# Optimization experiments

Measured on AMD Instinct MI355X. Metric: run time of the kernel, lower is better.

The kernel has to match this reference:

```python
import jax, jax.numpy as jnp
import numpy as np

ALPHA = 0.1
BETA = 0.3
MARGIN = 2.0


def setup_inputs() -> dict:
    key = jax.random.key(0)
    k1, k2 = jax.random.split(key)
    prediction = jax.random.normal(k1, (8, 2048, 512), dtype=jnp.float32)
    target_seg = jax.random.randint(k2, (8, 2048), 0, 16, dtype=jnp.int64)
    return {"prediction": prediction, "target_seg": target_seg}


def _pairwise_sqdist(x):
    # x: [n, L, d] -> squared Euclidean distances [n, L, L] via a GEMM
    sq = jnp.sum(x * x, axis=-1)  # [n, L]
    inner = jnp.einsum('nld,nmd->nlm', x, x)  # [n, L, L]
    d2 = sq[:, :, None] + sq[:, None, :] - 2.0 * inner
    return jnp.maximum(d2, 0.0)


def _safe_sqrt(d2):
    # sqrt with zero (not NaN) gradient at 0, matching torch.cdist behavior
    pos = d2 > 0
    return jnp.where(pos, jnp.sqrt(jnp.where(pos, d2, 1.0)), 0.0)


def reference(prediction, target_seg):
    # y[i,j,k] = 1 if target_seg[i,j] == target_seg[i,k]
    y = (target_seg[:, :, None] == target_seg[:, None, :]).astype(prediction.dtype)
    d2 = _pairwise_sqdist(prediction)
    dist = _safe_sqrt(d2)
    hinge = jnp.maximum(MARGIN - dist, 0.0)
    loss = ALPHA * y * d2 + BETA * (1.0 - y) * hinge * hinge
    return jnp.mean(loss)
```

## Files before the change

### kernel.cpp

```cpp
#include <hip/hip_runtime.h>
#include <hip/hip_fp8.h>
#include <math.h>

#define L      2048
#define DDIM   512
#define NBATCH 8
#define BM     128
#define BN     128
#define BK     128
#define NST    (DDIM / BK)
#define NTILE  (L / BM)
#define NPAIR  (NTILE * (NTILE + 1) / 2)
#define TOTAL_BLOCKS (NBATCH * NPAIR)

#define ALPHA  0.1f
#define BETA   0.3f
#define MARGIN 2.0f

typedef __attribute__((ext_vector_type(16))) float f32x16;
typedef _Float16 f16x8 __attribute__((ext_vector_type(8)));

#define BOFF   16384

#define GLOAD_LDS16(g, l) __builtin_amdgcn_global_load_lds(              \
    (const __attribute__((address_space(1))) unsigned int*)(g),          \
    (__attribute__((address_space(3))) unsigned int*)(l), 16, 0, 0)

__global__ __launch_bounds__(256) void conv_kernel(const float* __restrict__ pred,
                                                   unsigned char* __restrict__ h,
                                                   float* __restrict__ sq) {
    int w     = threadIdx.x >> 6;
    int lane  = threadIdx.x & 63;
    int batch = blockIdx.x & 7;
    int idx   = blockIdx.x >> 3;
    int row   = batch * L + idx * 4 + w;
    const float* p = pred + (size_t)row * DDIM + lane * 8;
    float4 v0 = *(const float4*)(p);
    float4 v1 = *(const float4*)(p + 4);
    float vals[8] = {v0.x, v0.y, v0.z, v0.w, v1.x, v1.y, v1.z, v1.w};
    unsigned q[8];
    float s = 0.0f;
    #pragma unroll
    for (int i = 0; i < 8; ++i) {
        float x = vals[i];
        s = fmaf(x, x, s);
        __hip_fp8_e4m3 f8(x);
        q[i] = (unsigned)f8.__x;
    }
    unsigned lo = q[0] | (q[1] << 8) | (q[2] << 16) | (q[3] << 24);
    unsigned hi = q[4] | (q[5] << 8) | (q[6] << 16) | (q[7] << 24);
    *(uint2*)(h + (size_t)row * DDIM + lane * 8) = make_uint2(lo, hi);
    #pragma unroll
    for (int off = 32; off > 0; off >>= 1) s += __shfl_down(s, off);
    if (lane == 0) sq[row] = s;
}

__global__ __launch_bounds__(256) void loss_kernel(
        const unsigned char* __restrict__ h,
        const int*   __restrict__ seg,
        const float* __restrict__ sq,
        double*      __restrict__ partials) {
    __shared__ unsigned char smem[32768];
    __shared__ double wred[4];

    int bid = blockIdx.x;
    int n = bid & 7;
    int p = bid >> 3;
    int tj = 0;
    while (true) {
        int rl2 = NTILE - tj;
        if (p < rl2) break;
        p -= rl2;
        ++tj;
    }
    int tk = tj + p;
    int j0 = tj * BM, k0 = tk * BN;

    int t    = threadIdx.x;
    int w    = t >> 6;
    int lane = t & 63;
    int wr   = w >> 1, wc = w & 1;
    int l31  = lane & 31;
    int hsel = lane >> 5;

    const unsigned char* baseH = h + (size_t)n * L * DDIM;

    int rl8 = lane >> 3;
    int lc  = (lane & 7) ^ rl8;
    const unsigned char* srcA = baseH + (size_t)(j0 + w * 32 + rl8) * DDIM + lc * 16;
    const unsigned char* srcB = baseH + (size_t)(k0 + w * 32 + rl8) * DDIM + lc * 16;
    unsigned char* dstA = smem + w * 4096;
    unsigned char* dstB = smem + BOFF + w * 4096;

    #define STAGE(st)                                                         \
    {                                                                         \
        _Pragma("unroll")                                                     \
        for (int q = 0; q < 4; ++q) {                                         \
            GLOAD_LDS16(srcA + (size_t)(q * 8) * DDIM + (st) * BK,            \
                        dstA + q * 1024);                                     \
            GLOAD_LDS16(srcB + (size_t)(q * 8) * DDIM + (st) * BK,            \
                        dstB + q * 1024);                                     \
        }                                                                     \
    }

    int s7  = l31 & 7;
    int rab = (wr * 64 + l31) * 128 + hsel * 8;
    int rbb = BOFF + (wc * 64 + l31) * 128 + hsel * 8;

    f32x16 acc[2][2];
    #pragma unroll
    for (int m = 0; m < 2; ++m)
        #pragma unroll
        for (int nn = 0; nn < 2; ++nn)
            #pragma unroll
            for (int r = 0; r < 16; ++r) acc[m][nn][r] = 0.0f;

    #pragma unroll
    for (int st = 0; st < NST; ++st) {
        __syncthreads();
        STAGE(st);
        __syncthreads();

        #pragma unroll
        for (int ks = 0; ks < 8; ++ks) {
            int xo = (ks ^ s7) << 4;
            long a0 = *(const long*)&smem[rab + xo];
            long a1 = *(const long*)&smem[rab + 4096 + xo];
            long b0 = *(const long*)&smem[rbb + xo];
            long b1 = *(const long*)&smem[rbb + 4096 + xo];
            acc[0][0] = __builtin_amdgcn_mfma_f32_32x32x16_fp8_fp8(a0, b0, acc[0][0], 0, 0, 0);
            acc[0][1] = __builtin_amdgcn_mfma_f32_32x32x16_fp8_fp8(a0, b1, acc[0][1], 0, 0, 0);
            acc[1][0] = __builtin_amdgcn_mfma_f32_32x32x16_fp8_fp8(a1, b0, acc[1][0], 0, 0, 0);
            acc[1][1] = __builtin_amdgcn_mfma_f32_32x32x16_fp8_fp8(a1, b1, acc[1][1], 0, 0, 0);
        }
    }

    const int*   segb = seg + n * L;
    const float* sqb  = sq + n * L;

    float lsum = 0.0f;
    #pragma unroll
    for (int nn = 0; nn < 2; ++nn) {
        int k = k0 + wc * 64 + nn * 32 + l31;
        float sqk = sqb[k];
        int   sgk = segb[k];
        #pragma unroll
        for (int m = 0; m < 2; ++m)
            #pragma unroll
            for (int r = 0; r < 16; ++r) {
                int j = j0 + wr * 64 + m * 32 + (r & 3) + 8 * (r >> 2) + 4 * hsel;
                float inner = acc[m][nn][r];
                float d2 = fmaxf(sqb[j] + sqk - 2.0f * inner, 0.0f);
                float v;
                if (segb[j] == sgk) {
                    v = ALPHA * d2;
                } else {
                    float dist = sqrtf(d2);
                    float hg = fmaxf(MARGIN - dist, 0.0f);
                    v = BETA * hg * hg;
                }
                lsum += v;
            }
    }

    double wgt = (tj == tk) ? 1.0 : 2.0;
    double dsum = (double)lsum * wgt;
    #pragma unroll
    for (int off = 32; off > 0; off >>= 1)
        dsum += __shfl_down(dsum, off);
    if (lane == 0) wred[w] = dsum;
    __syncthreads();
    if (t == 0) partials[bid] = (wred[0] + wred[1]) + (wred[2] + wred[3]);
}

__global__ __launch_bounds__(256) void reduce_kernel(const double* __restrict__ partials,
                                                     float* __restrict__ out,
                                                     int nPart, double invCount) {
    __shared__ double red[256];
    int t = threadIdx.x;
    double s = 0.0;
    for (int i = t; i < nPart; i += 256) s += partials[i];
    red[t] = s;
    __syncthreads();
    #pragma unroll
    for (int k = 128; k > 0; k >>= 1) {
        if (t < k) red[t] += red[t + k];
        __syncthreads();
    }
    if (t == 0) out[0] = (float)(red[0] * invCount);
}

extern "C" void kernel_launch(void* const* d_in, const int* in_sizes, int n_in,
                              void* d_out, int out_size, void* d_ws, size_t ws_size,
                              hipStream_t stream) {
    const float* pred = (const float*)d_in[0];
    const int*   seg  = (const int*)d_in[1];
    float* out = (float*)d_out;

    const size_t HALF = (size_t)NBATCH * L * DDIM;
    unsigned char* h  = (unsigned char*)d_ws;
    float*  sq        = (float*)(h + HALF);
    double* partials  = (double*)(sq + NBATCH * L);

    conv_kernel<<<NBATCH * L / 4, 256, 0, stream>>>(pred, h, sq);
    loss_kernel<<<TOTAL_BLOCKS, 256, 0, stream>>>(h, seg, sq, partials);
    reduce_kernel<<<1, 256, 0, stream>>>(partials, out, TOTAL_BLOCKS,
                                         1.0 / (double)((size_t)NBATCH * L * L));
}
```

Before: 55.84 us.

## Pack fp8 operands in MFMA-fragment panels and stream B directly from global

The conversion kernel now writes fp8 data in a pre-swizzled panel layout that matches the MFMA fragment order. Each loss block keeps one full 128-row A panel resident in LDS and loops over 4 column tiles, reading B fragments directly from global/L2 as 16-byte vectors. The triangular symmetry exploitation is dropped, so all 16x16 tile pairs are computed. This raises the total GEMM work by roughly 2x, in exchange for removing per-stage LDS staging and barriers and reusing A across tiles.

```diff
diff --git a/kernel.cpp b/kernel.cpp
--- a/kernel.cpp
+++ b/kernel.cpp
@@ -5,22 +5,17 @@
 #define L      2048
 #define DDIM   512
 #define NBATCH 8
-#define BM     128
-#define BN     128
-#define BK     128
-#define NST    (DDIM / BK)
-#define NTILE  (L / BM)
-#define NPAIR  (NTILE * (NTILE + 1) / 2)
-#define TOTAL_BLOCKS (NBATCH * NPAIR)
+#define NTJ    16
+#define TOTAL_BLOCKS (NBATCH * NTJ * 4)
+
+#define PANSZ  16384
 
 #define ALPHA  0.1f
 #define BETA   0.3f
 #define MARGIN 2.0f
 
 typedef __attribute__((ext_vector_type(16))) float f32x16;
-typedef _Float16 f16x8 __attribute__((ext_vector_type(8)));
-
-#define BOFF   16384
+typedef long long2v __attribute__((ext_vector_type(2)));
 
 #define GLOAD_LDS16(g, l) __builtin_amdgcn_global_load_lds(              \
     (const __attribute__((address_space(1))) unsigned int*)(g),          \
@@ -49,128 +44,118 @@
     }
     unsigned lo = q[0] | (q[1] << 8) | (q[2] << 16) | (q[3] << 24);
     unsigned hi = q[4] | (q[5] << 8) | (q[6] << 16) | (q[7] << 24);
-    *(uint2*)(h + (size_t)row * DDIM + lane * 8) = make_uint2(lo, hi);
+    int r5    = row & 31;
+    int pair  = lane >> 2;
+    int khalf = lane & 1;
+    int kodd  = (lane >> 1) & 1;
+    size_t off = (size_t)(row >> 5) * PANSZ + pair * 1024
+               + (r5 + 32 * khalf) * 16 + kodd * 8;
+    *(uint2*)(h + off) = make_uint2(lo, hi);
     #pragma unroll
-    for (int off = 32; off > 0; off >>= 1) s += __shfl_down(s, off);
+    for (int o = 32; o > 0; o >>= 1) s += __shfl_down(s, o);
     if (lane == 0) sq[row] = s;
 }
 
-__global__ __launch_bounds__(256) void loss_kernel(
+__global__ __launch_bounds__(256, 2) void loss_kernel(
         const unsigned char* __restrict__ h,
         const int*   __restrict__ seg,
         const float* __restrict__ sq,
         double*      __restrict__ partials) {
-    __shared__ unsigned char smem[32768];
-    __shared__ double wred[4];
+    __shared__ unsigned char As[65536];
 
     int bid = blockIdx.x;
-    int n = bid & 7;
-    int p = bid >> 3;
-    int tj = 0;
-    while (true) {
-        int rl2 = NTILE - tj;
-        if (p < rl2) break;
-        p -= rl2;
-        ++tj;
-    }
-    int tk = tj + p;
-    int j0 = tj * BM, k0 = tk * BN;
+    int n   = bid & 7;
+    int r   = bid >> 3;
+    int tj  = r >> 2;
+    int q4  = r & 3;
 
     int t    = threadIdx.x;
-    int w    = t >> 6;
+    int wid  = t >> 6;
     int lane = t & 63;
-    int wr   = w >> 1, wc = w & 1;
+    int wr   = wid >> 1;
+    int wn   = wid & 1;
     int l31  = lane & 31;
     int hsel = lane >> 5;
 
-    const unsigned char* baseH = h + (size_t)n * L * DDIM;
+    const unsigned char* base = h + (size_t)n * L * DDIM;
 
-    int rl8 = lane >> 3;
-    int lc  = (lane & 7) ^ rl8;
-    const unsigned char* srcA = baseH + (size_t)(j0 + w * 32 + rl8) * DDIM + lc * 16;
-    const unsigned char* srcB = baseH + (size_t)(k0 + w * 32 + rl8) * DDIM + lc * 16;
-    unsigned char* dstA = smem + w * 4096;
-    unsigned char* dstB = smem + BOFF + w * 4096;
-
-    #define STAGE(st)                                                         \
-    {                                                                         \
-        _Pragma("unroll")                                                     \
-        for (int q = 0; q < 4; ++q) {                                         \
-            GLOAD_LDS16(srcA + (size_t)(q * 8) * DDIM + (st) * BK,            \
-                        dstA + q * 1024);                                     \
-            GLOAD_LDS16(srcB + (size_t)(q * 8) * DDIM + (st) * BK,            \
-                        dstB + q * 1024);                                     \
-        }                                                                     \
+    {
+        const unsigned char* asrc = base + (size_t)(tj * 4 + wid) * PANSZ + lane * 16;
+        unsigned char* adst = As + wid * PANSZ;
+        #pragma unroll
+        for (int i = 0; i < 16; ++i)
+            GLOAD_LDS16(asrc + i * 1024, adst + i * 1024);
     }
-
-    int s7  = l31 & 7;
-    int rab = (wr * 64 + l31) * 128 + hsel * 8;
-    int rbb = BOFF + (wc * 64 + l31) * 128 + hsel * 8;
-
-    f32x16 acc[2][2];
-    #pragma unroll
-    for (int m = 0; m < 2; ++m)
-        #pragma unroll
-        for (int nn = 0; nn < 2; ++nn)
-            #pragma unroll
-            for (int r = 0; r < 16; ++r) acc[m][nn][r] = 0.0f;
-
-    #pragma unroll
-    for (int st = 0; st < NST; ++st) {
-        __syncthreads();
-        STAGE(st);
-        __syncthreads();
-
-        #pragma unroll
-        for (int ks = 0; ks < 8; ++ks) {
-            int xo = (ks ^ s7) << 4;
-            long a0 = *(const long*)&smem[rab + xo];
-            long a1 = *(const long*)&smem[rab + 4096 + xo];
-            long b0 = *(const long*)&smem[rbb + xo];
-            long b1 = *(const long*)&smem[rbb + 4096 + xo];
-            acc[0][0] = __builtin_amdgcn_mfma_f32_32x32x16_fp8_fp8(a0, b0, acc[0][0], 0, 0, 0);
-            acc[0][1] = __builtin_amdgcn_mfma_f32_32x32x16_fp8_fp8(a0, b1, acc[0][1], 0, 0, 0);
-            acc[1][0] = __builtin_amdgcn_mfma_f32_32x32x16_fp8_fp8(a1, b0, acc[1][0], 0, 0, 0);
-            acc[1][1] = __builtin_amdgcn_mfma_f32_32x32x16_fp8_fp8(a1, b1, acc[1][1], 0, 0, 0);
-        }
-    }
+    __syncthreads();
 
     const int*   segb = seg + n * L;
     const float* sqb  = sq + n * L;
 
     float lsum = 0.0f;
-    #pragma unroll
-    for (int nn = 0; nn < 2; ++nn) {
-        int k = k0 + wc * 64 + nn * 32 + l31;
-        float sqk = sqb[k];
-        int   sgk = segb[k];
+    int aoff0 = (wr * 2 + 0) * PANSZ + lane * 16;
+    int aoff1 = (wr * 2 + 1) * PANSZ + lane * 16;
+
+    #pragma unroll 1
+    for (int tkx = 0; tkx < 4; ++tkx) {
+        int tk = q4 * 4 + tkx;
+        const unsigned char* pb0 = base + (size_t)(tk * 4 + wn * 2) * PANSZ + lane * 16;
+        const unsigned char* pb1 = pb0 + PANSZ;
+
+        f32x16 acc[2][2];
         #pragma unroll
         for (int m = 0; m < 2; ++m)
             #pragma unroll
-            for (int r = 0; r < 16; ++r) {
-                int j = j0 + wr * 64 + m * 32 + (r & 3) + 8 * (r >> 2) + 4 * hsel;
-                float inner = acc[m][nn][r];
-                float d2 = fmaxf(sqb[j] + sqk - 2.0f * inner, 0.0f);
-                float v;
-                if (segb[j] == sgk) {
-                    v = ALPHA * d2;
-                } else {
-                    float dist = sqrtf(d2);
-                    float hg = fmaxf(MARGIN - dist, 0.0f);
-                    v = BETA * hg * hg;
+            for (int nf = 0; nf < 2; ++nf)
+                #pragma unroll
+                for (int x = 0; x < 16; ++x) acc[m][nf][x] = 0.0f;
+
+        #pragma unroll
+        for (int ks2 = 0; ks2 < 16; ++ks2) {
+            long2v a0 = *(const long2v*)&As[aoff0 + ks2 * 1024];
+            long2v a1 = *(const long2v*)&As[aoff1 + ks2 * 1024];
+            long2v b0 = *(const long2v*)(pb0 + ks2 * 1024);
+            long2v b1 = *(const long2v*)(pb1 + ks2 * 1024);
+            acc[0][0] = __builtin_amdgcn_mfma_f32_32x32x16_fp8_fp8(a0.x, b0.x, acc[0][0], 0, 0, 0);
+            acc[0][1] = __builtin_amdgcn_mfma_f32_32x32x16_fp8_fp8(a0.x, b1.x, acc[0][1], 0, 0, 0);
+            acc[1][0] = __builtin_amdgcn_mfma_f32_32x32x16_fp8_fp8(a1.x, b0.x, acc[1][0], 0, 0, 0);
+            acc[1][1] = __builtin_amdgcn_mfma_f32_32x32x16_fp8_fp8(a1.x, b1.x, acc[1][1], 0, 0, 0);
+            acc[0][0] = __builtin_amdgcn_mfma_f32_32x32x16_fp8_fp8(a0.y, b0.y, acc[0][0], 0, 0, 0);
+            acc[0][1] = __builtin_amdgcn_mfma_f32_32x32x16_fp8_fp8(a0.y, b1.y, acc[0][1], 0, 0, 0);
+            acc[1][0] = __builtin_amdgcn_mfma_f32_32x32x16_fp8_fp8(a1.y, b0.y, acc[1][0], 0, 0, 0);
+            acc[1][1] = __builtin_amdgcn_mfma_f32_32x32x16_fp8_fp8(a1.y, b1.y, acc[1][1], 0, 0, 0);
+        }
+
+        #pragma unroll
+        for (int nf = 0; nf < 2; ++nf) {
+            int k = tk * 128 + wn * 64 + nf * 32 + l31;
+            float sqk = sqb[k];
+            int   sgk = segb[k];
+            #pragma unroll
+            for (int m = 0; m < 2; ++m)
+                #pragma unroll
+                for (int x = 0; x < 16; ++x) {
+                    int j = tj * 128 + wr * 64 + m * 32
+                          + (x & 3) + 8 * (x >> 2) + 4 * hsel;
+                    float inner = acc[m][nf][x];
+                    float d2 = fmaxf(sqb[j] + sqk - 2.0f * inner, 0.0f);
+                    float v;
+                    if (segb[j] == sgk) {
+                        v = ALPHA * d2;
+                    } else {
+                        float dist = sqrtf(d2);
+                        float hg = fmaxf(MARGIN - dist, 0.0f);
+                        v = BETA * hg * hg;
+                    }
+                    lsum += v;
                 }
-                lsum += v;
-            }
+        }
     }
 
-    double wgt = (tj == tk) ? 1.0 : 2.0;
-    double dsum = (double)lsum * wgt;
+    double dsum = (double)lsum;
     #pragma unroll
     for (int off = 32; off > 0; off >>= 1)
         dsum += __shfl_down(dsum, off);
-    if (lane == 0) wred[w] = dsum;
-    __syncthreads();
-    if (t == 0) partials[bid] = (wred[0] + wred[1]) + (wred[2] + wred[3]);
+    if (lane == 0) partials[bid * 4 + wid] = dsum;
 }
 
 __global__ __launch_bounds__(256) void reduce_kernel(const double* __restrict__ partials,
@@ -204,6 +189,6 @@
 
     conv_kernel<<<NBATCH * L / 4, 256, 0, stream>>>(pred, h, sq);
     loss_kernel<<<TOTAL_BLOCKS, 256, 0, stream>>>(h, seg, sq, partials);
-    reduce_kernel<<<1, 256, 0, stream>>>(partials, out, TOTAL_BLOCKS,
+    reduce_kernel<<<1, 256, 0, stream>>>(partials, out, TOTAL_BLOCKS * 4,
                                          1.0 / (double)((size_t)NBATCH * L * L));
 }
```

Result: slower. 66.28 us (+18.7%).
